# Kernel optimization log

Measured on AMD Instinct MI355X. Metric: run time of the kernel, lower is better.

Reference implementation:

```python
import jax, jax.numpy as jnp
import numpy as np

B, T, I, H, O = 32, 512, 256, 1024, 512
TRUNC = 500


def _lstm_layer(x_seq, W_ih, W_hh, b_ih, b_hh):
    # x_seq: [T, B, in]; W_ih: [4H, in]; W_hh: [4H, H]
    # Precompute input contribution for the whole sequence (big GEMM).
    xg = jnp.einsum('tbi,gi->tbg', x_seq, W_ih) + b_ih + b_hh  # [T, B, 4H]
    Hd = W_hh.shape[1]
    h0 = jnp.zeros((x_seq.shape[1], Hd), x_seq.dtype)

    def step(carry, xg_t):
        h, c = carry
        gates = xg_t + h @ W_hh.T  # [B, 4H]
        i, f, g, o = jnp.split(gates, 4, axis=-1)  # PyTorch gate order i,f,g,o
        c = jax.nn.sigmoid(f) * c + jax.nn.sigmoid(i) * jnp.tanh(g)
        h = jax.nn.sigmoid(o) * jnp.tanh(c)
        return (h, c), h

    (_, _), hs = jax.lax.scan(step, (h0, h0), xg)
    return hs  # [T, B, H]


def setup_inputs() -> dict:
    key = jax.random.key(0)
    ks = jax.random.split(key, 12)
    s = 1.0 / np.sqrt(H)  # PyTorch uniform(-1/sqrt(H), 1/sqrt(H)) scale
    u = lambda k, shp: jax.random.uniform(k, shp, jnp.float32, -s, s)
    return {
        'x': jax.random.normal(ks[0], (B, T, I), jnp.float32),
        'W_ih0': u(ks[1], (4 * H, I)),
        'W_hh0': u(ks[2], (4 * H, H)),
        'b_ih0': u(ks[3], (4 * H,)),
        'b_hh0': u(ks[4], (4 * H,)),
        'W_ih1': u(ks[5], (4 * H, H)),
        'W_hh1': u(ks[6], (4 * H, H)),
        'b_ih1': u(ks[7], (4 * H,)),
        'b_hh1': u(ks[8], (4 * H,)),
        'W_fc': u(ks[9], (O, H)),
        'b_fc': u(ks[10], (O,)),
    }


def reference(x, W_ih0, W_hh0, b_ih0, b_hh0, W_ih1, W_hh1, b_ih1, b_hh1, W_fc, b_fc):
    xs = jnp.transpose(x, (1, 0, 2))  # [T, B, I] (time-major for scan)
    h1 = _lstm_layer(xs, W_ih0, W_hh0, b_ih0, b_hh0)
    h2 = _lstm_layer(h1, W_ih1, W_hh1, b_ih1, b_hh1)
    out = jnp.transpose(h2, (1, 0, 2))[:, :TRUNC, :]  # [B, 500, H]
    return jnp.einsum('bth,oh->bto', out, W_fc) + b_fc
```

## Files before the change

### kernel.cpp

```cpp
#include <hip/hip_runtime.h>
#include <cstdint>
#include <cstddef>


#define NTHR 512

typedef _Float16 f16;
typedef _Float16 f16x8 __attribute__((ext_vector_type(8)));
typedef float f32x4 __attribute__((ext_vector_type(4)));
typedef unsigned long long u64;

namespace {
constexpr int kT = 512, kI = 256, kH = 1024, kO = 512, kTR = 500;
constexpr int kSteps = 500;
constexpr size_t kHalfSlot = 32768;
constexpr size_t kTagL0 = 0;
constexpr size_t kTagL1 = 4096;
constexpr size_t kH1Off = 16384;
constexpr size_t kH2Off = kH1Off + 503ull * 2 * kHalfSlot;
constexpr int kRowH = 1048;
constexpr int kRowX = 264;
constexpr int kLdsBytes = 2 * 16 * kRowH * 2 + 4 * 16 * 17 * 4;
}

__device__ __forceinline__ unsigned ld_tag(const void* p) {
  return __hip_atomic_load((const unsigned*)p, __ATOMIC_RELAXED,
                           __HIP_MEMORY_SCOPE_AGENT);
}
__device__ __forceinline__ void st_tag(void* p, unsigned v) {
  __hip_atomic_store((unsigned*)p, v, __ATOMIC_RELAXED,
                     __HIP_MEMORY_SCOPE_AGENT);
}
__device__ __forceinline__ void st_rec_u64(void* p, u64 v) {
  __hip_atomic_store((u64*)p, v, __ATOMIC_RELAXED, __HIP_MEMORY_SCOPE_AGENT);
}
__device__ __forceinline__ float sigmoid_f(float x) {
  return __builtin_amdgcn_rcpf(1.f + __expf(-x));
}
__device__ __forceinline__ float tanh_f(float x) {
  return 1.f - 2.f * __builtin_amdgcn_rcpf(1.f + __expf(2.f * x));
}
__device__ __forceinline__ f16x8 load8(const float* p) {
  f16x8 r;
#pragma unroll
  for (int j = 0; j < 8; ++j) r[j] = (f16)p[j];
  return r;
}
__device__ __forceinline__ u64 pack4(float h, int lg) {
  f16 hv = (f16)h;
  unsigned short us;
  __builtin_memcpy(&us, &hv, 2);
  unsigned own = us;
  unsigned o1 = __shfl_xor((int)own, 16);
  unsigned p32 = (lg & 1) ? ((o1 & 0xffffu) | (own << 16))
                          : ((own & 0xffffu) | (o1 << 16));
  unsigned o2 = (unsigned)__shfl_xor((int)p32, 32);
  return (lg & 2) ? ((u64)o2 | ((u64)p32 << 32))
                  : ((u64)p32 | ((u64)o2 << 32));
}

__global__ void __launch_bounds__(256, 1) lstm_init_kernel(char* ws) {
  const int gid = blockIdx.x * 256 + threadIdx.x;
  unsigned* f = (unsigned*)ws;
  if (gid < 4096) f[gid] = 0u;
  u64* r1 = (u64*)(ws + kH1Off);
  u64* r2 = (u64*)(ws + kH2Off);
  if (gid < 8192) { r1[gid] = 0ull; r2[gid] = 0ull; }
}

__global__ void __launch_bounds__(NTHR, 1) __attribute__((amdgpu_waves_per_eu(2)))
lstm_pipe_kernel(const float* __restrict__ x,
                 const float* __restrict__ Wih0, const float* __restrict__ Whh0,
                 const float* __restrict__ bih0, const float* __restrict__ bhh0,
                 const float* __restrict__ Wih1, const float* __restrict__ Whh1,
                 const float* __restrict__ bih1, const float* __restrict__ bhh1,
                 const float* __restrict__ Wfc, const float* __restrict__ bfc,
                 float* __restrict__ out, char* __restrict__ ws) {
  const int tid = threadIdx.x;
  const int bk = blockIdx.x;
  const int w = tid >> 6;
  const int lane = tid & 63;
  const int m = lane & 15;
  const int kg = lane >> 4;
  const int lg = lane >> 4;
  const int c = bk & 7, rho = bk >> 3;
  extern __shared__ char smem[];

  if (c < 2) {
    const int half = c;
    const int q = m >> 2, g = m & 3;
    const int uA = rho * 32 + 4 * w + q;
    const int uD = rho * 32 + 4 * w + lg;
    f16x8 whh[32], wih[8];
#pragma unroll
    for (int kc = 0; kc < 32; ++kc)
      whh[kc] = load8(Whh0 + (size_t)(g * kH + uA) * kH + kc * 32 + kg * 8);
#pragma unroll
    for (int kx = 0; kx < 8; ++kx)
      wih[kx] = load8(Wih0 + (size_t)(g * kH + uA) * kI + kx * 32 + kg * 8);
    float bias[4];
#pragma unroll
    for (int j = 0; j < 4; ++j) bias[j] = bih0[j * kH + uD] + bhh0[j * kH + uD];
    float cst = 0.f;
    f16* ldsH = (f16*)smem;
    f16* ldsX = (f16*)(smem + 16 * kRowH * 2);
    unsigned* tagMy = (unsigned*)(ws + kTagL0 + (size_t)half * 2048);
    const int xb = tid >> 5, xcol = (tid & 31) * 8;
    const int sb = tid >> 7, so = (tid & 127) * 8;

    for (int t = 1; t <= kSteps; ++t) {
      if (w == 7) {
        const unsigned tgt = (unsigned)(t - 1);
        const unsigned* tp = tagMy + (size_t)(lane & 31) * 16;
        bool done;
        do {
          done = __all((int)(ld_tag(tp) >= tgt));
          if (!done) __builtin_amdgcn_s_sleep(1);
        } while (!done);
      }
      {
        f16x8 xv = load8(x + ((size_t)(half * 16 + xb) * kT + (t - 1)) * kI + xcol);
        *(f16x8*)(ldsX + xb * kRowX + xcol) = xv;
      }
      __syncthreads();
      {
        const char* rec = ws + kH1Off + ((size_t)(t - 1) * 2 + half) * kHalfSlot;
        f16x8 h0 = *(const f16x8*)(rec + (size_t)tid * 16);
        f16x8 h1v = *(const f16x8*)(rec + (size_t)(tid + 512) * 16);
        f16x8 h2v = *(const f16x8*)(rec + (size_t)(tid + 1024) * 16);
        f16x8 h3v = *(const f16x8*)(rec + (size_t)(tid + 1536) * 16);
        *(f16x8*)(ldsH + (sb + 0) * kRowH + so) = h0;
        *(f16x8*)(ldsH + (sb + 4) * kRowH + so) = h1v;
        *(f16x8*)(ldsH + (sb + 8) * kRowH + so) = h2v;
        *(f16x8*)(ldsH + (sb + 12) * kRowH + so) = h3v;
      }
      __syncthreads();
      f32x4 acc = {0.f, 0.f, 0.f, 0.f};
#pragma unroll
      for (int kc = 0; kc < 32; ++kc) {
        f16x8 bf = *(const f16x8*)(ldsH + m * kRowH + kc * 32 + kg * 8);
        acc = __builtin_amdgcn_mfma_f32_16x16x32_f16(whh[kc], bf, acc, 0, 0, 0);
      }
#pragma unroll
      for (int kx = 0; kx < 8; ++kx) {
        f16x8 bf = *(const f16x8*)(ldsX + m * kRowX + kx * 32 + kg * 8);
        acc = __builtin_amdgcn_mfma_f32_16x16x32_f16(wih[kx], bf, acc, 0, 0, 0);
      }
      const float pi = acc[0] + bias[0], pf = acc[1] + bias[1];
      const float pg = acc[2] + bias[2], po = acc[3] + bias[3];
      cst = sigmoid_f(pf) * cst + sigmoid_f(pi) * tanh_f(pg);
      const float h = sigmoid_f(po) * tanh_f(cst);
      const u64 pk = pack4(h, lg);
      if (lane < 16) {
        st_rec_u64(ws + kH1Off + ((size_t)t * 2 + half) * kHalfSlot +
                       (size_t)lane * 2048 + (size_t)(rho * 32 + 4 * w) * 2,
                   pk);
        asm volatile("s_waitcnt vmcnt(0)" ::: "memory");
      }
      __syncthreads();
      if (tid == 0) st_tag(tagMy + (size_t)rho * 16, (unsigned)t);
    }

  } else if (c < 6) {
    const int half = c & 1;
    const int rank = rho + ((c >= 4) ? 32 : 0);
    const int u0 = rank * 16;
    const int rg = w & 3, kh = w >> 2;
    const int q = m >> 2, g = m & 3;
    const int uA = u0 + 4 * rg + q;
    const int uD = u0 + 4 * rg + lg;
    const float* WA = kh ? Whh1 : Wih1;
    f16x8 wa[32];
#pragma unroll
    for (int kc = 0; kc < 32; ++kc)
      wa[kc] = load8(WA + (size_t)(g * kH + uA) * kH + kc * 32 + kg * 8);
    float bias[4];
#pragma unroll
    for (int j = 0; j < 4; ++j) bias[j] = bih1[j * kH + uD] + bhh1[j * kH + uD];
    float cst = 0.f;
    f16* ldsH1 = (f16*)smem;
    f16* ldsH2 = (f16*)(smem + 16 * kRowH * 2);
    float* zone = (float*)(smem + 2 * 16 * kRowH * 2);
    unsigned* tagL0h = (unsigned*)(ws + kTagL0 + (size_t)half * 2048);
    unsigned* tagL1h = (unsigned*)(ws + kTagL1 + (size_t)half * 4096);
    const int sb = tid >> 7, so = (tid & 127) * 8;

    for (int t = 1; t <= kSteps; ++t) {
      if (w == 7) {
        const unsigned tgtA = (unsigned)t, tgtB = (unsigned)(t - 1);
        const unsigned* tpB = tagL1h + (size_t)lane * 16;
        const unsigned* tpA = tagL0h + (size_t)(lane & 31) * 16;
        bool done;
        do {
          bool ok = (ld_tag(tpB) >= tgtB);
          if (lane < 32) ok = ok && (ld_tag(tpA) >= tgtA);
          done = __all((int)ok);
          if (!done) __builtin_amdgcn_s_sleep(1);
        } while (!done);
      }
      __syncthreads();
      {
        const char* r1 = ws + kH1Off + ((size_t)t * 2 + half) * kHalfSlot;
        const char* r2 = ws + kH2Off + ((size_t)(t - 1) * 2 + half) * kHalfSlot;
        f16x8 a0 = *(const f16x8*)(r1 + (size_t)tid * 16);
        f16x8 a1 = *(const f16x8*)(r1 + (size_t)(tid + 512) * 16);
        f16x8 a2 = *(const f16x8*)(r1 + (size_t)(tid + 1024) * 16);
        f16x8 a3 = *(const f16x8*)(r1 + (size_t)(tid + 1536) * 16);
        f16x8 b0 = *(const f16x8*)(r2 + (size_t)tid * 16);
        f16x8 b1 = *(const f16x8*)(r2 + (size_t)(tid + 512) * 16);
        f16x8 b2 = *(const f16x8*)(r2 + (size_t)(tid + 1024) * 16);
        f16x8 b3 = *(const f16x8*)(r2 + (size_t)(tid + 1536) * 16);
        *(f16x8*)(ldsH1 + (sb + 0) * kRowH + so) = a0;
        *(f16x8*)(ldsH1 + (sb + 4) * kRowH + so) = a1;
        *(f16x8*)(ldsH1 + (sb + 8) * kRowH + so) = a2;
        *(f16x8*)(ldsH1 + (sb + 12) * kRowH + so) = a3;
        *(f16x8*)(ldsH2 + (sb + 0) * kRowH + so) = b0;
        *(f16x8*)(ldsH2 + (sb + 4) * kRowH + so) = b1;
        *(f16x8*)(ldsH2 + (sb + 8) * kRowH + so) = b2;
        *(f16x8*)(ldsH2 + (sb + 12) * kRowH + so) = b3;
      }
      __syncthreads();
      const f16* ldsB = kh ? ldsH2 : ldsH1;
      f32x4 acc = {0.f, 0.f, 0.f, 0.f};
#pragma unroll
      for (int kc = 0; kc < 32; ++kc) {
        f16x8 bf = *(const f16x8*)(ldsB + m * kRowH + kc * 32 + kg * 8);
        acc = __builtin_amdgcn_mfma_f32_16x16x32_f16(wa[kc], bf, acc, 0, 0, 0);
      }
      if (kh == 0) {
#pragma unroll
        for (int j = 0; j < 4; ++j)
          zone[(rg * 16 + lg * 4 + j) * 17 + m] = acc[j];
      }
      __syncthreads();
      if (kh == 1) {
        const float pi = acc[0] + zone[(rg * 16 + lg * 4 + 0) * 17 + m] + bias[0];
        const float pf = acc[1] + zone[(rg * 16 + lg * 4 + 1) * 17 + m] + bias[1];
        const float pg = acc[2] + zone[(rg * 16 + lg * 4 + 2) * 17 + m] + bias[2];
        const float po = acc[3] + zone[(rg * 16 + lg * 4 + 3) * 17 + m] + bias[3];
        cst = sigmoid_f(pf) * cst + sigmoid_f(pi) * tanh_f(pg);
        const float h = sigmoid_f(po) * tanh_f(cst);
        const u64 pk = pack4(h, lg);
        if (lane < 16) {
          st_rec_u64(ws + kH2Off + ((size_t)t * 2 + half) * kHalfSlot +
                         (size_t)lane * 2048 + (size_t)(u0 + 4 * rg) * 2,
                     pk);
          asm volatile("s_waitcnt vmcnt(0)" ::: "memory");
        }
      }
      __syncthreads();
      if (tid == 0) st_tag(tagL1h + (size_t)rank * 16, (unsigned)t);
    }

  } else {
    const int half = c - 6;
    const int o0 = rho * 16;
    f16x8 wf[4];
#pragma unroll
    for (int i = 0; i < 4; ++i)
      wf[i] = load8(Wfc + (size_t)(o0 + m) * kH + (size_t)(w + 8 * i) * 32 + kg * 8);
    f16* ldsH = (f16*)smem;
    float* zone = (float*)(smem + 16 * kRowH * 2);
    unsigned* tagL1h = (unsigned*)(ws + kTagL1 + (size_t)half * 4096);
    const int sb = tid >> 7, so = (tid & 127) * 8;
    const int ob = lane >> 2, op = lane & 3;
    float4 bf4;
    if (w == 0) bf4 = *(const float4*)(bfc + o0 + op * 4);

    for (int t = 1; t <= kSteps; ++t) {
      if (w == 7) {
        const unsigned tgt = (unsigned)t;
        const unsigned* tp = tagL1h + (size_t)lane * 16;
        bool done;
        do {
          done = __all((int)(ld_tag(tp) >= tgt));
          if (!done) __builtin_amdgcn_s_sleep(1);
        } while (!done);
      }
      __syncthreads();
      {
        const char* r2 = ws + kH2Off + ((size_t)t * 2 + half) * kHalfSlot;
        f16x8 b0 = *(const f16x8*)(r2 + (size_t)tid * 16);
        f16x8 b1 = *(const f16x8*)(r2 + (size_t)(tid + 512) * 16);
        f16x8 b2 = *(const f16x8*)(r2 + (size_t)(tid + 1024) * 16);
        f16x8 b3 = *(const f16x8*)(r2 + (size_t)(tid + 1536) * 16);
        *(f16x8*)(ldsH + (sb + 0) * kRowH + so) = b0;
        *(f16x8*)(ldsH + (sb + 4) * kRowH + so) = b1;
        *(f16x8*)(ldsH + (sb + 8) * kRowH + so) = b2;
        *(f16x8*)(ldsH + (sb + 12) * kRowH + so) = b3;
      }
      __syncthreads();
      f32x4 acc = {0.f, 0.f, 0.f, 0.f};
#pragma unroll
      for (int i = 0; i < 4; ++i) {
        f16x8 bf = *(const f16x8*)(ldsH + m * kRowH + (w + 8 * i) * 32 + kg * 8);
        acc = __builtin_amdgcn_mfma_f32_16x16x32_f16(wf[i], bf, acc, 0, 0, 0);
      }
#pragma unroll
      for (int j = 0; j < 4; ++j)
        zone[(w * 16 + lg * 4 + j) * 17 + m] = acc[j];
      __syncthreads();
      if (w == 0) {
        float4 v;
#pragma unroll
        for (int jj = 0; jj < 4; ++jj) {
          float s = 0.f;
#pragma unroll
          for (int ww = 0; ww < 8; ++ww)
            s += zone[(ww * 16 + op * 4 + jj) * 17 + ob];
          ((float*)&v)[jj] = s + ((const float*)&bf4)[jj];
        }
        *(float4*)(out + ((size_t)(half * 16 + ob) * kTR + (t - 1)) * kO +
                   o0 + op * 4) = v;
      }
    }
  }
}

extern "C" void kernel_launch(void* const* d_in, const int* in_sizes, int n_in,
                              void* d_out, int out_size, void* d_ws,
                              size_t ws_size, hipStream_t stream) {
  const float* x    = (const float*)d_in[0];
  const float* Wih0 = (const float*)d_in[1];
  const float* Whh0 = (const float*)d_in[2];
  const float* bih0 = (const float*)d_in[3];
  const float* bhh0 = (const float*)d_in[4];
  const float* Wih1 = (const float*)d_in[5];
  const float* Whh1 = (const float*)d_in[6];
  const float* bih1 = (const float*)d_in[7];
  const float* bhh1 = (const float*)d_in[8];
  const float* Wfc  = (const float*)d_in[9];
  const float* bfc  = (const float*)d_in[10];
  float* out = (float*)d_out;
  char* ws   = (char*)d_ws;

  (void)hipFuncSetAttribute((const void*)lstm_pipe_kernel,
                            hipFuncAttributeMaxDynamicSharedMemorySize,
                            kLdsBytes);

  hipLaunchKernelGGL(lstm_init_kernel, dim3(128), dim3(256), 0, stream, ws);
  hipLaunchKernelGGL(lstm_pipe_kernel, dim3(256), dim3(NTHR), kLdsBytes,
                     stream, x, Wih0, Whh0, bih0, bhh0, Wih1, Whh1, bih1,
                     bhh1, Wfc, bfc, out, ws);
}
```

Before: 2.400 ms.

## Replace per-block completion barrier with per-wave tags and double-buffer x tile

Each wave now publishes its own completion tag after draining its stores, instead of a block-wide __syncthreads followed by a single tag from thread 0. Pollers read the per-wave tags with 64-bit loads and check all of them. The x input tile for layer 0 is double-buffered and loaded before the wait so the global load overlaps the polling, and the LDS row paddings change. This removes one block barrier per step on the recurrent critical path, at the cost of more tag traffic and a more complex readiness check.

```diff
diff --git a/kernel.cpp b/kernel.cpp
--- a/kernel.cpp
+++ b/kernel.cpp
@@ -18,13 +18,15 @@
 constexpr size_t kTagL1 = 4096;
 constexpr size_t kH1Off = 16384;
 constexpr size_t kH2Off = kH1Off + 503ull * 2 * kHalfSlot;
-constexpr int kRowH = 1048;
-constexpr int kRowX = 264;
-constexpr int kLdsBytes = 2 * 16 * kRowH * 2 + 4 * 16 * 17 * 4;
-}
-
-__device__ __forceinline__ unsigned ld_tag(const void* p) {
-  return __hip_atomic_load((const unsigned*)p, __ATOMIC_RELAXED,
+constexpr int kRowH = 1034;
+constexpr int kRowX = 266;
+constexpr int kHBytes = 16 * kRowH * 2;
+constexpr int kXBytes = 16 * kRowX * 2;
+constexpr int kLdsBytes = 2 * kHBytes + 4 * 16 * 17 * 4;
+}
+
+__device__ __forceinline__ u64 ld_tag64(const void* p) {
+  return __hip_atomic_load((const u64*)p, __ATOMIC_RELAXED,
                            __HIP_MEMORY_SCOPE_AGENT);
 }
 __device__ __forceinline__ void st_tag(void* p, unsigned v) {
@@ -33,6 +35,10 @@
 }
 __device__ __forceinline__ void st_rec_u64(void* p, u64 v) {
   __hip_atomic_store((u64*)p, v, __ATOMIC_RELAXED, __HIP_MEMORY_SCOPE_AGENT);
+}
+__device__ __forceinline__ bool tag4_ge(u64 a, u64 b, unsigned t) {
+  return ((unsigned)a >= t) && ((unsigned)(a >> 32) >= t) &&
+         ((unsigned)b >= t) && ((unsigned)(b >> 32) >= t);
 }
 __device__ __forceinline__ float sigmoid_f(float x) {
   return __builtin_amdgcn_rcpf(1.f + __expf(-x));
@@ -103,24 +109,29 @@
     for (int j = 0; j < 4; ++j) bias[j] = bih0[j * kH + uD] + bhh0[j * kH + uD];
     float cst = 0.f;
     f16* ldsH = (f16*)smem;
-    f16* ldsX = (f16*)(smem + 16 * kRowH * 2);
-    unsigned* tagMy = (unsigned*)(ws + kTagL0 + (size_t)half * 2048);
+    f16* ldsX0 = (f16*)(smem + kHBytes);
+    f16* ldsX1 = (f16*)(smem + kHBytes + kXBytes);
+    char* tagLine = ws + kTagL0 + (size_t)half * 2048 + (size_t)rho * 64;
+    const u64* tpoll = (const u64*)(ws + kTagL0 + (size_t)half * 2048 +
+                                    (size_t)(lane >> 1) * 64 +
+                                    (size_t)(lane & 1) * 16);
     const int xb = tid >> 5, xcol = (tid & 31) * 8;
     const int sb = tid >> 7, so = (tid & 127) * 8;
 
     for (int t = 1; t <= kSteps; ++t) {
-      if (w == 7) {
-        const unsigned tgt = (unsigned)(t - 1);
-        const unsigned* tp = tagMy + (size_t)(lane & 31) * 16;
-        bool done;
-        do {
-          done = __all((int)(ld_tag(tp) >= tgt));
-          if (!done) __builtin_amdgcn_s_sleep(1);
-        } while (!done);
-      }
+      f16* ldsX = (t & 1) ? ldsX1 : ldsX0;
       {
         f16x8 xv = load8(x + ((size_t)(half * 16 + xb) * kT + (t - 1)) * kI + xcol);
         *(f16x8*)(ldsX + xb * kRowX + xcol) = xv;
+      }
+      if (w == 7) {
+        const unsigned tgt = (unsigned)(t - 1);
+        bool done;
+        do {
+          u64 a = ld_tag64(tpoll), b = ld_tag64(tpoll + 1);
+          done = __all((int)tag4_ge(a, b, tgt));
+          if (!done) __builtin_amdgcn_s_sleep(1);
+        } while (!done);
       }
       __syncthreads();
       {
@@ -155,10 +166,9 @@
         st_rec_u64(ws + kH1Off + ((size_t)t * 2 + half) * kHalfSlot +
                        (size_t)lane * 2048 + (size_t)(rho * 32 + 4 * w) * 2,
                    pk);
-        asm volatile("s_waitcnt vmcnt(0)" ::: "memory");
-      }
-      __syncthreads();
-      if (tid == 0) st_tag(tagMy + (size_t)rho * 16, (unsigned)t);
+      }
+      asm volatile("s_waitcnt vmcnt(0)" ::: "memory");
+      if (lane == 0) st_tag(tagLine + w * 4, (unsigned)t);
     }
 
   } else if (c < 6) {
@@ -179,21 +189,26 @@
     for (int j = 0; j < 4; ++j) bias[j] = bih1[j * kH + uD] + bhh1[j * kH + uD];
     float cst = 0.f;
     f16* ldsH1 = (f16*)smem;
-    f16* ldsH2 = (f16*)(smem + 16 * kRowH * 2);
-    float* zone = (float*)(smem + 2 * 16 * kRowH * 2);
-    unsigned* tagL0h = (unsigned*)(ws + kTagL0 + (size_t)half * 2048);
-    unsigned* tagL1h = (unsigned*)(ws + kTagL1 + (size_t)half * 4096);
+    f16* ldsH2 = (f16*)(smem + kHBytes);
+    float* zone = (float*)(smem + 2 * kHBytes);
+    char* tagLine = ws + kTagL1 + (size_t)half * 4096 + (size_t)rank * 64;
+    const u64* tpB = (const u64*)(ws + kTagL1 + (size_t)half * 4096 +
+                                  (size_t)lane * 64);
+    const u64* tpA = (const u64*)(ws + kTagL0 + (size_t)half * 2048 +
+                                  (size_t)(lane >> 1) * 64 +
+                                  (size_t)(lane & 1) * 16);
     const int sb = tid >> 7, so = (tid & 127) * 8;
 
     for (int t = 1; t <= kSteps; ++t) {
       if (w == 7) {
         const unsigned tgtA = (unsigned)t, tgtB = (unsigned)(t - 1);
-        const unsigned* tpB = tagL1h + (size_t)lane * 16;
-        const unsigned* tpA = tagL0h + (size_t)(lane & 31) * 16;
         bool done;
         do {
-          bool ok = (ld_tag(tpB) >= tgtB);
-          if (lane < 32) ok = ok && (ld_tag(tpA) >= tgtA);
+          u64 b0 = ld_tag64(tpB);
+          u64 b1 = ld_tag64(tpB + 1);
+          u64 a0 = ld_tag64(tpA);
+          u64 a1 = ld_tag64(tpA + 1);
+          bool ok = tag4_ge(b0, b1, tgtB) && tag4_ge(a0, a1, tgtA);
           done = __all((int)ok);
           if (!done) __builtin_amdgcn_s_sleep(1);
         } while (!done);
@@ -245,11 +260,10 @@
           st_rec_u64(ws + kH2Off + ((size_t)t * 2 + half) * kHalfSlot +
                          (size_t)lane * 2048 + (size_t)(u0 + 4 * rg) * 2,
                      pk);
-          asm volatile("s_waitcnt vmcnt(0)" ::: "memory");
         }
-      }
-      __syncthreads();
-      if (tid == 0) st_tag(tagL1h + (size_t)rank * 16, (unsigned)t);
+        asm volatile("s_waitcnt vmcnt(0)" ::: "memory");
+        if (lane == 0) st_tag(tagLine + (w - 4) * 4, (unsigned)t);
+      }
     }
 
   } else {
@@ -260,8 +274,9 @@
     for (int i = 0; i < 4; ++i)
       wf[i] = load8(Wfc + (size_t)(o0 + m) * kH + (size_t)(w + 8 * i) * 32 + kg * 8);
     f16* ldsH = (f16*)smem;
-    float* zone = (float*)(smem + 16 * kRowH * 2);
-    unsigned* tagL1h = (unsigned*)(ws + kTagL1 + (size_t)half * 4096);
+    float* zone = (float*)(smem + kHBytes);
+    const u64* tpB = (const u64*)(ws + kTagL1 + (size_t)half * 4096 +
+                                  (size_t)lane * 64);
     const int sb = tid >> 7, so = (tid & 127) * 8;
     const int ob = lane >> 2, op = lane & 3;
     float4 bf4;
@@ -270,10 +285,10 @@
     for (int t = 1; t <= kSteps; ++t) {
       if (w == 7) {
         const unsigned tgt = (unsigned)t;
-        const unsigned* tp = tagL1h + (size_t)lane * 16;
         bool done;
         do {
-          done = __all((int)(ld_tag(tp) >= tgt));
+          u64 b0 = ld_tag64(tpB), b1 = ld_tag64(tpB + 1);
+          done = __all((int)tag4_ge(b0, b1, tgt));
           if (!done) __builtin_amdgcn_s_sleep(1);
         } while (!done);
       }
```

New measurement: 6.466 ms. 2.69x slower.

## Split layer-1 step so the recurrent GEMM overlaps fetching layer-0 output

Applied to the files above, without the earlier changes.

The layer-1 step loop no longer waits for layer 0 and layer 1 tags together. It first waits only on the previous layer-1 hidden state and stages it in LDS. The wait on layer 0's tag for step t moves later, just before that staging store. The recurrent half-warps then run W_hh·h2 while the input half-warps load h1 from global memory into LDS. After that the input half-warps run W_ih·h1 and the gate/cell update. This is meant to hide part of the layer-0 dependency latency behind the recurrent matmul. In exchange the two MFMA chains now run one after the other instead of side by side, and the cell state moves to the other warp group.

```diff
diff --git a/kernel.cpp b/kernel.cpp
--- a/kernel.cpp
+++ b/kernel.cpp
@@ -187,53 +187,66 @@
 
     for (int t = 1; t <= kSteps; ++t) {
       if (w == 7) {
-        const unsigned tgtA = (unsigned)t, tgtB = (unsigned)(t - 1);
+        const unsigned tgtB = (unsigned)(t - 1);
         const unsigned* tpB = tagL1h + (size_t)lane * 16;
-        const unsigned* tpA = tagL0h + (size_t)(lane & 31) * 16;
         bool done;
         do {
-          bool ok = (ld_tag(tpB) >= tgtB);
-          if (lane < 32) ok = ok && (ld_tag(tpA) >= tgtA);
-          done = __all((int)ok);
+          done = __all((int)(ld_tag(tpB) >= tgtB));
           if (!done) __builtin_amdgcn_s_sleep(1);
         } while (!done);
       }
       __syncthreads();
       {
-        const char* r1 = ws + kH1Off + ((size_t)t * 2 + half) * kHalfSlot;
         const char* r2 = ws + kH2Off + ((size_t)(t - 1) * 2 + half) * kHalfSlot;
-        f16x8 a0 = *(const f16x8*)(r1 + (size_t)tid * 16);
-        f16x8 a1 = *(const f16x8*)(r1 + (size_t)(tid + 512) * 16);
-        f16x8 a2 = *(const f16x8*)(r1 + (size_t)(tid + 1024) * 16);
-        f16x8 a3 = *(const f16x8*)(r1 + (size_t)(tid + 1536) * 16);
         f16x8 b0 = *(const f16x8*)(r2 + (size_t)tid * 16);
         f16x8 b1 = *(const f16x8*)(r2 + (size_t)(tid + 512) * 16);
         f16x8 b2 = *(const f16x8*)(r2 + (size_t)(tid + 1024) * 16);
         f16x8 b3 = *(const f16x8*)(r2 + (size_t)(tid + 1536) * 16);
-        *(f16x8*)(ldsH1 + (sb + 0) * kRowH + so) = a0;
-        *(f16x8*)(ldsH1 + (sb + 4) * kRowH + so) = a1;
-        *(f16x8*)(ldsH1 + (sb + 8) * kRowH + so) = a2;
-        *(f16x8*)(ldsH1 + (sb + 12) * kRowH + so) = a3;
+        if (w == 7) {
+          const unsigned tgtA = (unsigned)t;
+          const unsigned* tpA = tagL0h + (size_t)(lane & 31) * 16;
+          bool done;
+          do {
+            done = __all((int)(ld_tag(tpA) >= tgtA));
+            if (!done) __builtin_amdgcn_s_sleep(1);
+          } while (!done);
+        }
         *(f16x8*)(ldsH2 + (sb + 0) * kRowH + so) = b0;
         *(f16x8*)(ldsH2 + (sb + 4) * kRowH + so) = b1;
         *(f16x8*)(ldsH2 + (sb + 8) * kRowH + so) = b2;
         *(f16x8*)(ldsH2 + (sb + 12) * kRowH + so) = b3;
       }
       __syncthreads();
-      const f16* ldsB = kh ? ldsH2 : ldsH1;
-      f32x4 acc = {0.f, 0.f, 0.f, 0.f};
-#pragma unroll
-      for (int kc = 0; kc < 32; ++kc) {
-        f16x8 bf = *(const f16x8*)(ldsB + m * kRowH + kc * 32 + kg * 8);
-        acc = __builtin_amdgcn_mfma_f32_16x16x32_f16(wa[kc], bf, acc, 0, 0, 0);
-      }
-      if (kh == 0) {
+      if (kh == 1) {
+        f32x4 acc = {0.f, 0.f, 0.f, 0.f};
+#pragma unroll
+        for (int kc = 0; kc < 32; ++kc) {
+          f16x8 bf = *(const f16x8*)(ldsH2 + m * kRowH + kc * 32 + kg * 8);
+          acc = __builtin_amdgcn_mfma_f32_16x16x32_f16(wa[kc], bf, acc, 0, 0, 0);
+        }
 #pragma unroll
         for (int j = 0; j < 4; ++j)
           zone[(rg * 16 + lg * 4 + j) * 17 + m] = acc[j];
-      }
-      __syncthreads();
-      if (kh == 1) {
+      } else {
+        const char* r1 = ws + kH1Off + ((size_t)t * 2 + half) * kHalfSlot;
+        f16x8 a[8];
+#pragma unroll
+        for (int j = 0; j < 8; ++j)
+          a[j] = *(const f16x8*)(r1 + ((size_t)(j * 256 + tid)) * 16);
+#pragma unroll
+        for (int j = 0; j < 8; ++j) {
+          const int i = j * 256 + tid;
+          *(f16x8*)(ldsH1 + (i >> 7) * kRowH + (i & 127) * 8) = a[j];
+        }
+      }
+      __syncthreads();
+      if (kh == 0) {
+        f32x4 acc = {0.f, 0.f, 0.f, 0.f};
+#pragma unroll
+        for (int kc = 0; kc < 32; ++kc) {
+          f16x8 bf = *(const f16x8*)(ldsH1 + m * kRowH + kc * 32 + kg * 8);
+          acc = __builtin_amdgcn_mfma_f32_16x16x32_f16(wa[kc], bf, acc, 0, 0, 0);
+        }
         const float pi = acc[0] + zone[(rg * 16 + lg * 4 + 0) * 17 + m] + bias[0];
         const float pf = acc[1] + zone[(rg * 16 + lg * 4 + 1) * 17 + m] + bias[1];
         const float pg = acc[2] + zone[(rg * 16 + lg * 4 + 2) * 17 + m] + bias[2];
```

After: 2.281 ms. 4.9% less time.
